# Kernel tuning notes

Hardware: AMD Instinct MI355X
Metric: run time of the kernel (lower is better)

## Reference

```python
import jax, jax.numpy as jnp
import numpy as np

B, C, H, W, K = 4, 96, 56, 56, 9
CM = 2 * C  # graph-conv output channels (standard Grapher: 2*in_channels)


def setup_inputs() -> dict:
    key = jax.random.key(0)
    ks = jax.random.split(key, 6)
    x = jax.random.normal(ks[0], (B, C, H, W), jnp.float32)
    fc1_w = jax.random.normal(ks[1], (C, C), jnp.float32) * 0.05
    fc1_b = jnp.zeros((C,), jnp.float32)
    gconv_w = jax.random.normal(ks[2], (CM, 2 * C), jnp.float32) * 0.05
    gconv_b = jnp.zeros((CM,), jnp.float32)
    fc2_w = jax.random.normal(ks[3], (C, CM), jnp.float32) * 0.05
    fc2_b = jnp.zeros((C,), jnp.float32)
    sa_w = jax.random.normal(ks[4], (1, 2, 7, 7), jnp.float32) * 0.05
    return dict(x=x, fc1_w=fc1_w, fc1_b=fc1_b, gconv_w=gconv_w, gconv_b=gconv_b,
                fc2_w=fc2_w, fc2_b=fc2_b, sa_w=sa_w)


def _knn_idx(xf, k):
    # xf: (B, C, N) -> (B, N, k) nearest-neighbor indices (includes self),
    # matching dense_knn_matrix: topk of negative squared euclidean distance.
    x2 = jnp.sum(xf * xf, axis=1)                       # (B, N)
    inner = jnp.einsum('bcn,bcm->bnm', xf, xf)          # (B, N, N)
    dist = x2[:, :, None] - 2.0 * inner + x2[:, None, :]
    _, idx = jax.lax.top_k(-dist, k)                    # (B, N, k)
    return idx


def _grapher(x, fc1_w, fc1_b, gconv_w, gconv_b, fc2_w, fc2_b, sa_w):
    shortcut = x
    # fc1: 1x1 conv C -> C
    h = jnp.einsum('bchw,oc->bohw', x, fc1_w) + fc1_b[None, :, None, None]
    b, c, hh, ww = h.shape
    n = hh * ww
    xf = h.reshape(b, c, n)                              # nodes: (B, C, N)
    idx = _knn_idx(xf, K)                                # dynamic KNN graph
    # EdgeConv2d: gather x_j at neighbor indices, x_i = center
    xt = jnp.transpose(xf, (0, 2, 1))                    # (B, N, C)
    x_j = jax.vmap(lambda t, i: t[i])(xt, idx)           # (B, N, K, C)
    x_j = jnp.transpose(x_j, (0, 3, 1, 2))               # (B, C, N, K)
    x_i = xf[:, :, :, None]                              # (B, C, N, 1)
    feat = jnp.concatenate(
        [jnp.broadcast_to(x_i, x_j.shape), x_j - x_i], axis=1)  # (B, 2C, N, K)
    e = jnp.einsum('bcnk,oc->bonk', feat, gconv_w) + gconv_b[None, :, None, None]
    e = jax.nn.relu(e)
    g = jnp.max(e, axis=-1)                              # max over K neighbors
    g = g.reshape(b, CM, hh, ww)
    # fc2: 1x1 conv 2C -> C
    out = jnp.einsum('bchw,oc->bohw', g, fc2_w) + fc2_b[None, :, None, None]
    # SpatialAttention: channel mean/max -> 7x7 conv -> sigmoid gate
    avg = jnp.mean(out, axis=1, keepdims=True)
    mx = jnp.max(out, axis=1, keepdims=True)
    sa_in = jnp.concatenate([avg, mx], axis=1)           # (B, 2, H, W)
    att = jax.lax.conv_general_dilated(
        sa_in, sa_w, window_strides=(1, 1), padding=[(3, 3), (3, 3)],
        dimension_numbers=('NCHW', 'OIHW', 'NCHW'))
    att = jax.nn.sigmoid(att)
    return out * att + shortcut


def reference(x, fc1_w, fc1_b, gconv_w, gconv_b, fc2_w, fc2_b, sa_w):
    return _grapher(x, fc1_w, fc1_b, gconv_w, gconv_b, fc2_w, fc2_b, sa_w)
```

## Files before the change

kernel.cpp:

```cpp
#include <hip/hip_runtime.h>

#define BB 4
#define CC 96
#define NN 3136
#define FLTMAX 3.402823466e+38f
#define CAP 44
#define DELTA 1.0f

typedef unsigned short ushort_t;
typedef __attribute__((ext_vector_type(8))) short bf16x8;
typedef __attribute__((ext_vector_type(4))) float f32x4;

__device__ __forceinline__ ushort_t f2bf(float f) {
    unsigned u = __float_as_uint(f);
    unsigned r = (u + 0x7fff + ((u >> 16) & 1)) >> 16;
    return (ushort_t)r;
}
__device__ __forceinline__ float bf2f(ushort_t us) {
    return __uint_as_float(((unsigned)us) << 16);
}


__global__ __launch_bounds__(256) void k_fc1(const float* __restrict__ x, const float* __restrict__ w,
                                             const float* __restrict__ bias, float* __restrict__ h,
                                             float* __restrict__ x2g,
                                             ushort_t* __restrict__ hAhi,
                                             float* __restrict__ hT) {
    __shared__ float sm[96 * 98 + 96 * 64];
    float* wT = sm;
    float* xl = sm + 96 * 98;
    const int tid = threadIdx.x;
    const int n0 = blockIdx.x * 64;
    const int b = blockIdx.y;
    for (int i = tid; i < 96 * 96; i += 256) {
        int o = i / 96, c = i - o * 96;
        wT[c * 98 + o] = w[i];
    }
    const float* xb = x + (size_t)b * CC * NN;
    for (int i = tid; i < 96 * 64; i += 256) {
        int c = i >> 6, nl = i & 63;
        xl[i] = xb[(size_t)c * NN + n0 + nl];
    }
    __syncthreads();
    const int tr = tid >> 4, tc = tid & 15;
    float acc[6][4];
#pragma unroll
    for (int i = 0; i < 6; ++i)
#pragma unroll
        for (int j = 0; j < 4; ++j) acc[i][j] = 0.f;
#pragma unroll 4
    for (int c = 0; c < 96; ++c) {
        float4 xv = *(const float4*)&xl[c * 64 + tc * 4];
        const float* wp = &wT[c * 98 + tr * 6];
        float2 w01 = *(const float2*)(wp);
        float2 w23 = *(const float2*)(wp + 2);
        float2 w45 = *(const float2*)(wp + 4);
        float wv[6] = {w01.x, w01.y, w23.x, w23.y, w45.x, w45.y};
        float xj[4] = {xv.x, xv.y, xv.z, xv.w};
#pragma unroll
        for (int i = 0; i < 6; ++i)
#pragma unroll
            for (int j = 0; j < 4; ++j) acc[i][j] = fmaf(wv[i], xj[j], acc[i][j]);
    }
    float* hb = h + (size_t)b * CC * NN;
    float* hTb = hT + (size_t)b * NN * 96;
    ushort_t* thi = hAhi + (size_t)b * 602112;
#pragma unroll
    for (int i = 0; i < 6; ++i) {
        float bi = bias[tr * 6 + i];
        acc[i][0] += bi; acc[i][1] += bi; acc[i][2] += bi; acc[i][3] += bi;
        float4 o4 = make_float4(acc[i][0], acc[i][1], acc[i][2], acc[i][3]);
        *(float4*)&hb[(size_t)(tr * 6 + i) * NN + n0 + tc * 4] = o4;
        const int c = tr * 6 + i;
        const int cpart = c >> 3;
#pragma unroll
        for (int j = 0; j < 4; ++j) {
            const int n = n0 + tc * 4 + j;
            const int idx = (((n >> 5) * 12 + cpart) * 32 + (n & 31)) * 8 + (c & 7);
            thi[idx] = f2bf(acc[i][j]);
            hTb[(size_t)n * 96 + c] = acc[i][j];
        }
    }
    __syncthreads();
#pragma unroll
    for (int j = 0; j < 4; ++j) {
        float s = 0.f;
#pragma unroll
        for (int i = 0; i < 6; ++i) s = fmaf(acc[i][j], acc[i][j], s);
        sm[tr * 64 + tc * 4 + j] = s;
    }
    __syncthreads();
    if (tid < 64) {
        float s = 0.f;
#pragma unroll
        for (int t = 0; t < 16; ++t) s += sm[t * 64 + tid];
        x2g[(size_t)b * NN + n0 + tid] = s;
    }
}

#define MFMA_TILE_HI(t, acc0, acc1, acc2, acc3)                                       \
    {                                                                                 \
        const int abase_ = (t) * 6144;                                                \
        _Pragma("unroll")                                                             \
        for (int ks_ = 0; ks_ < 3; ++ks_) {                                           \
            const int base_ = abase_ + ks_ * 1024;                                    \
            bf16x8 a0_ = *(const bf16x8*)(hHi + base_ + aoff0);                       \
            bf16x8 a1_ = *(const bf16x8*)(hHi + base_ + aoff1);                       \
            bf16x8 a2_ = *(const bf16x8*)(hHi + base_ + 3072 + aoff0);                \
            bf16x8 a3_ = *(const bf16x8*)(hHi + base_ + 3072 + aoff1);                \
            acc0 = __builtin_amdgcn_mfma_f32_16x16x32_bf16(a0_, bhi[ks_], acc0, 0, 0, 0); \
            acc1 = __builtin_amdgcn_mfma_f32_16x16x32_bf16(a1_, bhi[ks_], acc1, 0, 0, 0); \
            acc2 = __builtin_amdgcn_mfma_f32_16x16x32_bf16(a2_, bhi[ks_], acc2, 0, 0, 0); \
            acc3 = __builtin_amdgcn_mfma_f32_16x16x32_bf16(a3_, bhi[ks_], acc3, 0, 0, 0); \
        }                                                                             \
    }

__global__ __launch_bounds__(256) void k_dist(const ushort_t* __restrict__ hAhi,
                                              const float* __restrict__ x2,
                                              int* __restrict__ cand_cnt,
                                              int* __restrict__ cand_idx,
                                              float* __restrict__ thr_row) {
    __shared__ float thrb[32][24];
    __shared__ float thr_s[32];
    __shared__ int   cnt[32];
    __shared__ int   list[32][CAP];
    const int tid = threadIdx.x;
    const int nb = blockIdx.x, q = blockIdx.y, b = blockIdx.z;
    const int w = tid >> 6, l = tid & 63;
    const int ln = l & 15, lq = l >> 4;
    const int p = w >> 1;
    const int kl_off = lq * 256;
    const ushort_t* hHi = hAhi + (size_t)b * 602112;
    const float* x2b = x2 + (size_t)b * NN;

    const int lane32n = (w & 1) * 16 + ln;
    bf16x8 bhi[3];
#pragma unroll
    for (int ks = 0; ks < 3; ++ks) {
        const int off = nb * 3072 + ks * 1024 + kl_off + lane32n * 8;
        bhi[ks] = *(const bf16x8*)(hHi + off);
    }
    const int aoff0 = kl_off + ln * 8;
    const int aoff1 = kl_off + (16 + ln) * 8;

    const int qb0 = (q == 0) ? 0 : (q == 1) ? 13 : (q == 2) ? 25 : 37;
    const int qb1 = (q == 0) ? 13 : (q == 1) ? 25 : (q == 2) ? 37 : 49;
    const int tstart = qb0 + p;

    unsigned scache[7][8];
    float lv0 = FLTMAX, lv1 = FLTMAX, lv2 = FLTMAX;
#pragma unroll
    for (int ti = 0; ti < 7; ++ti) {
        const int t = tstart + 2 * ti;
        if (t < qb1) {
            const int m0 = t * 64;
            f32x4 acc0 = {0.f, 0.f, 0.f, 0.f}, acc1 = {0.f, 0.f, 0.f, 0.f};
            f32x4 acc2 = {0.f, 0.f, 0.f, 0.f}, acc3 = {0.f, 0.f, 0.f, 0.f};
            MFMA_TILE_HI(t, acc0, acc1, acc2, acc3);
#pragma unroll
            for (int msub = 0; msub < 4; ++msub) {
                f32x4 a = (msub == 0) ? acc0 : (msub == 1) ? acc1 : (msub == 2) ? acc2 : acc3;
                const int mb = m0 + msub * 16 + lq * 4;
                float4 xv = *(const float4*)&x2b[mb];
                float s0 = fmaf(-2.f, a[0], xv.x);
                float s1 = fmaf(-2.f, a[1], xv.y);
                float s2 = fmaf(-2.f, a[2], xv.z);
                float s3 = fmaf(-2.f, a[3], xv.w);
                scache[ti][msub * 2 + 0] = ((unsigned)f2bf(s0) << 16) | (unsigned)f2bf(s1);
                scache[ti][msub * 2 + 1] = ((unsigned)f2bf(s2) << 16) | (unsigned)f2bf(s3);
                float ss[4] = {s0, s1, s2, s3};
#pragma unroll
                for (int r = 0; r < 4; ++r) {
                    float v = ss[r];
                    float t0 = fminf(lv0, v);
                    lv0 = fmaxf(t0, lv1);
                    float t1 = fminf(t0, lv1);
                    lv1 = fmaxf(t1, lv2);
                    lv2 = fminf(t1, lv2);
                }
            }
        }
    }
    {
        const int sidx = (p * 4 + lq) * 3;
        thrb[lane32n][sidx + 0] = lv0;
        thrb[lane32n][sidx + 1] = lv1;
        thrb[lane32n][sidx + 2] = lv2;
    }
    __syncthreads();
    if (tid < 32) {
        float tmp[24];
#pragma unroll
        for (int j = 0; j < 24; ++j) tmp[j] = thrb[tid][j];
        float last = FLTMAX;
        for (int kk = 0; kk < 9; ++kk) {
            float mn = FLTMAX; int ms = 0;
            for (int j = 0; j < 24; ++j)
                if (tmp[j] < mn) { mn = tmp[j]; ms = j; }
            tmp[ms] = FLTMAX;
            last = mn;
        }
        thr_s[tid] = last + DELTA;
        cnt[tid] = 0;
        thr_row[((size_t)b * NN + nb * 32 + tid) * 4 + q] = last + DELTA;
    }
    __syncthreads();
    const float thr = thr_s[lane32n];

#pragma unroll
    for (int ti = 0; ti < 7; ++ti) {
        const int t = tstart + 2 * ti;
        if (t < qb1) {
            const int m0 = t * 64;
#pragma unroll
            for (int msub = 0; msub < 4; ++msub) {
                const int mb = m0 + msub * 16 + lq * 4;
                const unsigned u01 = scache[ti][msub * 2 + 0];
                const unsigned u23 = scache[ti][msub * 2 + 1];
                unsigned bits[4] = {u01 >> 16, u01 & 0xffffu, u23 >> 16, u23 & 0xffffu};
#pragma unroll
                for (int r = 0; r < 4; ++r) {
                    if (bf2f((ushort_t)bits[r]) <= thr) {
                        int pos = atomicAdd(&cnt[lane32n], 1);
                        if (pos < CAP) list[lane32n][pos] = (int)((bits[r] << 16) | (unsigned)(mb + r));
                    }
                }
            }
        }
    }
    __syncthreads();
    const size_t rowbase = (size_t)b * NN + nb * 32;
    if (tid < 32) cand_cnt[(rowbase + tid) * 4 + q] = min(cnt[tid], CAP);
    for (int i = tid; i < 32 * CAP; i += 256) {
        int r = i / CAP, j = i - r * CAP;
        if (j < min(cnt[r], CAP))
            cand_idx[((rowbase + r) * 4 + q) * CAP + j] = list[r][j];
    }
}

__global__ __launch_bounds__(256) void k_merge9(const int* __restrict__ cand_cnt,
                                                const int* __restrict__ cand_idx,
                                                const float* __restrict__ thr_row,
                                                const float* __restrict__ hT,
                                                const float* __restrict__ x2,
                                                int* __restrict__ idx9) {
    __shared__ int  np[4];
    __shared__ int2 pl[4][192];
    const int tid = threadIdx.x;
    const int wv = tid >> 6, lane = tid & 63;
    const size_t n = (size_t)blockIdx.x * 4 + wv;
    const int b = (int)(n / NN);
    const int nn = (int)(n - (size_t)b * NN);
    const int c0 = cand_cnt[n * 4 + 0];
    const int c1 = cand_cnt[n * 4 + 1];
    const int c2 = cand_cnt[n * 4 + 2];
    const int c3 = cand_cnt[n * 4 + 3];
    const int p1 = c0, p2 = c0 + c1, p3 = c0 + c1 + c2;
    const int ct = p3 + c3;
    const float cutoff = fminf(fminf(thr_row[n * 4 + 0], thr_row[n * 4 + 1]),
                               fminf(thr_row[n * 4 + 2], thr_row[n * 4 + 3]));
    if (lane == 0) np[wv] = 0;
    const float* hTb = hT + (size_t)b * NN * 96;
    const float* own = hTb + (size_t)nn * 96;
    const float* x2b = x2 + (size_t)b * NN;
#pragma unroll
    for (int t = 0; t < 3; ++t) {
        const int j = lane + 64 * t;
        if (j < ct) {
            const int qq = (j >= p1) + (j >= p2) + (j >= p3);
            const int base = (qq == 0) ? 0 : (qq == 1) ? p1 : (qq == 2) ? p2 : p3;
            const unsigned u = (unsigned)cand_idx[(n * 4 + qq) * CAP + (j - base)];
            const float av = bf2f((ushort_t)(u >> 16));
            if (av <= cutoff) {
                const int cj = (int)(u & 0xffffu);
                const float* cr = hTb + (size_t)cj * 96;
                float dot = 0.f;
#pragma unroll
                for (int i = 0; i < 24; ++i) {
                    float4 rv = *(const float4*)&own[i * 4];
                    float4 cv4 = *(const float4*)&cr[i * 4];
                    dot = fmaf(rv.x, cv4.x, dot);
                    dot = fmaf(rv.y, cv4.y, dot);
                    dot = fmaf(rv.z, cv4.z, dot);
                    dot = fmaf(rv.w, cv4.w, dot);
                }
                const float v = fmaf(-2.f, dot, x2b[cj]);
                const int pos = atomicAdd(&np[wv], 1);
                pl[wv][pos] = make_int2(__float_as_int(v), cj);
            }
        }
    }
    const int npw = np[wv];
    int2 mine[3]; int rk[3];
#pragma unroll
    for (int t = 0; t < 3; ++t) {
        const int s = lane + 64 * t;
        mine[t] = (s < npw) ? pl[wv][s] : make_int2(0x7f7fffff, 0x7fffffff);
        rk[t] = 0;
    }
    for (int j2 = 0; j2 < npw; ++j2) {
        const int2 e = pl[wv][j2];
        const float ev = __int_as_float(e.x);
#pragma unroll
        for (int t = 0; t < 3; ++t) {
            const float mv = __int_as_float(mine[t].x);
            rk[t] += (ev < mv || (ev == mv && e.y < mine[t].y)) ? 1 : 0;
        }
    }
    int* dst = idx9 + n * 9;
#pragma unroll
    for (int t = 0; t < 3; ++t) {
        const int s = lane + 64 * t;
        if (s < npw && rk[t] < 9) dst[rk[t]] = mine[t].y;
    }
}

__global__ __launch_bounds__(256) void k_ac(const float* __restrict__ h, const float* __restrict__ gw,
                                            const float* __restrict__ gb, ushort_t* __restrict__ acT) {
    __shared__ float sm[96 * 98 + 96 * 64];
    float* wT = sm;
    float* hl = sm + 96 * 98;
    const int tid = threadIdx.x;
    const int n0 = blockIdx.x * 64, ot = blockIdx.y, b = blockIdx.z;
    for (int i = tid; i < 96 * 96; i += 256) {
        int o = i / 96, c = i - o * 96;
        float v;
        if (ot < 2) {
            const float* gwp = gw + (size_t)(ot * 96 + o) * 192;
            v = gwp[c] - gwp[96 + c];
        } else {
            v = gw[(size_t)((ot - 2) * 96 + o) * 192 + 96 + c];
        }
        wT[c * 98 + o] = v;
    }
    const float* hb = h + (size_t)b * CC * NN;
    for (int i = tid; i < 96 * 64; i += 256) {
        int c = i >> 6, nl = i & 63;
        hl[i] = hb[(size_t)c * NN + n0 + nl];
    }
    __syncthreads();
    const int tr = tid >> 4, tc = tid & 15;
    float acc[6][4];
#pragma unroll
    for (int i = 0; i < 6; ++i)
#pragma unroll
        for (int j = 0; j < 4; ++j) acc[i][j] = 0.f;
#pragma unroll 4
    for (int c = 0; c < 96; ++c) {
        float4 xv = *(const float4*)&hl[c * 64 + tc * 4];
        const float* wp = &wT[c * 98 + tr * 6];
        float2 w01 = *(const float2*)(wp);
        float2 w23 = *(const float2*)(wp + 2);
        float2 w45 = *(const float2*)(wp + 4);
        float wv[6] = {w01.x, w01.y, w23.x, w23.y, w45.x, w45.y};
        float xj[4] = {xv.x, xv.y, xv.z, xv.w};
#pragma unroll
        for (int i = 0; i < 6; ++i)
#pragma unroll
            for (int j = 0; j < 4; ++j) acc[i][j] = fmaf(wv[i], xj[j], acc[i][j]);
    }
    const int obase = ot * 96 + tr * 6;
    float bs[6];
#pragma unroll
    for (int i = 0; i < 6; ++i) bs[i] = (ot < 2) ? gb[obase + i] : 0.f;
#pragma unroll
    for (int j = 0; j < 4; ++j) {
        ushort_t* dst = acT + ((size_t)b * NN + n0 + tc * 4 + j) * 384 + obase;
        ushort2 p0, p1, p2;
        p0.x = f2bf(acc[0][j] + bs[0]); p0.y = f2bf(acc[1][j] + bs[1]);
        p1.x = f2bf(acc[2][j] + bs[2]); p1.y = f2bf(acc[3][j] + bs[3]);
        p2.x = f2bf(acc[4][j] + bs[4]); p2.y = f2bf(acc[5][j] + bs[5]);
        *(ushort2*)(dst + 0) = p0;
        *(ushort2*)(dst + 2) = p1;
        *(ushort2*)(dst + 4) = p2;
    }
}

__global__ __launch_bounds__(256) void k_gather(const ushort_t* __restrict__ acT,
                                                const int* __restrict__ idx9,
                                                float* __restrict__ gT) {
    const int lane = threadIdx.x & 63;
    const int wv = threadIdx.x >> 6;
    const int b = blockIdx.y;
    const int nb = blockIdx.x * 16 + wv * 4;
    for (int r = 0; r < 4; ++r) {
        const int n = nb + r;
        const ushort_t* ar = acT + ((size_t)b * NN + n) * 384;
        float a0 = bf2f(ar[lane]), a1 = bf2f(ar[lane + 64]), a2 = bf2f(ar[lane + 128]);
        const int* ip = idx9 + ((size_t)b * NN + n) * 9;
        int jj[9];
#pragma unroll
        for (int k = 0; k < 9; ++k) jj[k] = ip[k];
        float m0 = -FLTMAX, m1 = -FLTMAX, m2 = -FLTMAX;
#pragma unroll
        for (int k = 0; k < 9; ++k) {
            const ushort_t* cr = acT + ((size_t)b * NN + jj[k]) * 384 + 192;
            m0 = fmaxf(m0, a0 + bf2f(cr[lane]));
            m1 = fmaxf(m1, a1 + bf2f(cr[lane + 64]));
            m2 = fmaxf(m2, a2 + bf2f(cr[lane + 128]));
        }
        float* gr = gT + ((size_t)b * NN + n) * 192;
        gr[lane] = fmaxf(m0, 0.f);
        gr[lane + 64] = fmaxf(m1, 0.f);
        gr[lane + 128] = fmaxf(m2, 0.f);
    }
}

__global__ __launch_bounds__(256) void k_fc2(const float* __restrict__ gT, const float* __restrict__ w,
                                             const float* __restrict__ bias, float* __restrict__ out,
                                             float* __restrict__ sa_in) {
    __shared__ float Wc[96 * 36];
    __shared__ float Gc[16 * 36];
    __shared__ float red[2][16][17];
    const int tid = threadIdx.x;
    const int n0 = blockIdx.x * 16, b = blockIdx.y;
    const int tr = tid >> 4, tc = tid & 15;
    float acc[6];
#pragma unroll
    for (int i = 0; i < 6; ++i) acc[i] = 0.f;
    for (int kc = 0; kc < 192; kc += 32) {
        for (int i = tid; i < 96 * 32; i += 256) {
            int c = i >> 5, k = i & 31;
            Wc[c * 36 + k] = w[(size_t)c * 192 + kc + k];
        }
        for (int i = tid; i < 16 * 32; i += 256) {
            int nl = i >> 5, k = i & 31;
            Gc[nl * 36 + k] = gT[((size_t)b * NN + n0 + nl) * 192 + kc + k];
        }
        __syncthreads();
#pragma unroll
        for (int k = 0; k < 32; k += 4) {
            float4 gv = *(const float4*)&Gc[tc * 36 + k];
#pragma unroll
            for (int i = 0; i < 6; ++i) {
                float4 wv = *(const float4*)&Wc[(tr * 6 + i) * 36 + k];
                acc[i] = fmaf(wv.x, gv.x, acc[i]);
                acc[i] = fmaf(wv.y, gv.y, acc[i]);
                acc[i] = fmaf(wv.z, gv.z, acc[i]);
                acc[i] = fmaf(wv.w, gv.w, acc[i]);
            }
        }
        __syncthreads();
    }
    float* ob = out + (size_t)b * CC * NN;
    float ps = 0.f, pm = -FLTMAX;
#pragma unroll
    for (int i = 0; i < 6; ++i) {
        float o = acc[i] + bias[tr * 6 + i];
        ob[(size_t)(tr * 6 + i) * NN + n0 + tc] = o;
        ps += o;
        pm = fmaxf(pm, o);
    }
    red[0][tr][tc] = ps;
    red[1][tr][tc] = pm;
    __syncthreads();
    if (tid < 16) {
        float s_ = 0.f, m_ = -FLTMAX;
#pragma unroll
        for (int t = 0; t < 16; ++t) { s_ += red[0][t][tid]; m_ = fmaxf(m_, red[1][t][tid]); }
        sa_in[(size_t)b * 2 * NN + n0 + tid] = s_ * (1.0f / 96.0f);
        sa_in[(size_t)b * 2 * NN + NN + n0 + tid] = m_;
    }
}

__global__ __launch_bounds__(256) void k_att(const float* __restrict__ sa_in, const float* __restrict__ sw,
                                             const float* __restrict__ x, float* __restrict__ out) {
    int n = blockIdx.x * 256 + threadIdx.x;
    int b = blockIdx.y;
    if (n >= NN) return;
    int y = n / 56, xw = n - y * 56;
    float acc = 0.f;
#pragma unroll
    for (int ci = 0; ci < 2; ++ci) {
        const float* sb = sa_in + ((size_t)b * 2 + ci) * NN;
#pragma unroll
        for (int dy = 0; dy < 7; ++dy) {
            int yy = y + dy - 3;
            if ((unsigned)yy < 56u) {
#pragma unroll
                for (int dx = 0; dx < 7; ++dx) {
                    int xx = xw + dx - 3;
                    if ((unsigned)xx < 56u)
                        acc = fmaf(sb[yy * 56 + xx], sw[(ci * 7 + dy) * 7 + dx], acc);
                }
            }
        }
    }
    float att = 1.f / (1.f + expf(-acc));
    const float* xb = x + (size_t)b * CC * NN + n;
    float* ob = out + (size_t)b * CC * NN + n;
#pragma unroll 4
    for (int c = 0; c < 96; ++c) {
        size_t o = (size_t)c * NN;
        ob[o] = fmaf(ob[o], att, xb[o]);
    }
}

extern "C" void kernel_launch(void* const* d_in, const int* in_sizes, int n_in,
                              void* d_out, int out_size, void* d_ws, size_t ws_size,
                              hipStream_t stream) {
    (void)in_sizes; (void)n_in; (void)out_size; (void)ws_size;
    const float* x       = (const float*)d_in[0];
    const float* fc1_w   = (const float*)d_in[1];
    const float* fc1_b   = (const float*)d_in[2];
    const float* gconv_w = (const float*)d_in[3];
    const float* gconv_b = (const float*)d_in[4];
    const float* fc2_w   = (const float*)d_in[5];
    const float* fc2_b   = (const float*)d_in[6];
    const float* sa_w    = (const float*)d_in[7];
    float* out = (float*)d_out;

    float* ws   = (float*)d_ws;
    float* h    = ws;
    float* x2   = h + (size_t)BB * CC * NN;
    int*   idx9 = (int*)(x2 + BB * NN);
    float* regA = (float*)(idx9 + (size_t)BB * NN * 9);
    ushort_t* hAhi = (ushort_t*)regA;
    ushort_t* acT  = (ushort_t*)regA;
    float* hT   = regA + 2408448;
    float* regB = hT + 1204224;
    int*   cand_idx = (int*)regB;
    int*   cand_cnt = (int*)(regB + 2207744);
    float* thr_row  = regB + 2207744 + 50176;
    float* gT   = regB;
    float* sa_in = regB + 2408448;

    k_fc1   <<<dim3(49, BB), 256, 0, stream>>>(x, fc1_w, fc1_b, h, x2, hAhi, hT);
    k_dist  <<<dim3(98, 4, BB), 256, 0, stream>>>(hAhi, x2, cand_cnt, cand_idx, thr_row);
    k_merge9<<<dim3(3136), 256, 0, stream>>>(cand_cnt, cand_idx, thr_row, hT, x2, idx9);
    k_ac    <<<dim3(49, 4, BB), 256, 0, stream>>>(h, gconv_w, gconv_b, acT);
    k_gather<<<dim3(196, BB), 256, 0, stream>>>(acT, idx9, gT);
    k_fc2   <<<dim3(196, BB), 256, 0, stream>>>(gT, fc2_w, fc2_b, out, sa_in);
    k_att   <<<dim3(13, BB), 256, 0, stream>>>(sa_in, sa_w, x, out);
}
```

Baseline: 248.2 us.

## Split candidate distance dot products across four lanes in KNN merge

The merge kernel now first compacts the surviving candidate indices into shared memory, then recomputes their distances with four lanes per candidate. Each lane handles 24 channels and the partial sums are combined with xor shuffles. Previously each active lane serially read a full 96-float row, which gave divergent, poorly coalesced loads. The change adds block-wide barriers and a loop bounded by the largest wave's candidate count, so waves with fewer candidates sit idle through extra iterations.

```diff
diff --git a/kernel.cpp b/kernel.cpp
--- a/kernel.cpp
+++ b/kernel.cpp
@@ -245,7 +245,8 @@
                                                 const float* __restrict__ x2,
                                                 int* __restrict__ idx9) {
     __shared__ int  np[4];
-    __shared__ int2 pl[4][192];
+    __shared__ int  cl[4][192];
+    __shared__ int2 vl[4][192];
     const int tid = threadIdx.x;
     const int wv = tid >> 6, lane = tid & 63;
     const size_t n = (size_t)blockIdx.x * 4 + wv;
@@ -260,9 +261,7 @@
     const float cutoff = fminf(fminf(thr_row[n * 4 + 0], thr_row[n * 4 + 1]),
                                fminf(thr_row[n * 4 + 2], thr_row[n * 4 + 3]));
     if (lane == 0) np[wv] = 0;
-    const float* hTb = hT + (size_t)b * NN * 96;
-    const float* own = hTb + (size_t)nn * 96;
-    const float* x2b = x2 + (size_t)b * NN;
+    __syncthreads();
 #pragma unroll
     for (int t = 0; t < 3; ++t) {
         const int j = lane + 64 * t;
@@ -272,34 +271,57 @@
             const unsigned u = (unsigned)cand_idx[(n * 4 + qq) * CAP + (j - base)];
             const float av = bf2f((ushort_t)(u >> 16));
             if (av <= cutoff) {
-                const int cj = (int)(u & 0xffffu);
-                const float* cr = hTb + (size_t)cj * 96;
-                float dot = 0.f;
-#pragma unroll
-                for (int i = 0; i < 24; ++i) {
-                    float4 rv = *(const float4*)&own[i * 4];
-                    float4 cv4 = *(const float4*)&cr[i * 4];
-                    dot = fmaf(rv.x, cv4.x, dot);
-                    dot = fmaf(rv.y, cv4.y, dot);
-                    dot = fmaf(rv.z, cv4.z, dot);
-                    dot = fmaf(rv.w, cv4.w, dot);
-                }
-                const float v = fmaf(-2.f, dot, x2b[cj]);
                 const int pos = atomicAdd(&np[wv], 1);
-                pl[wv][pos] = make_int2(__float_as_int(v), cj);
+                cl[wv][pos] = (int)(u & 0xffffu);
             }
         }
     }
+    __syncthreads();
     const int npw = np[wv];
+    const int npmax = max(max(np[0], np[1]), max(np[2], np[3]));
+    const float* hTb = hT + (size_t)b * NN * 96;
+    const float* x2b = x2 + (size_t)b * NN;
+    const int part = lane & 3, slot = lane >> 2;
+    float4 ro[6];
+    {
+        const float* own = hTb + (size_t)nn * 96 + part * 24;
+#pragma unroll
+        for (int i = 0; i < 6; ++i) ro[i] = *(const float4*)&own[i * 4];
+    }
+    for (int base = 0; base < npmax; base += 16) {
+        const int s = base + slot;
+        const bool act = (s < npw);
+        int cj = 0;
+        float dot = 0.f;
+        if (act) {
+            cj = cl[wv][s];
+            const float* cr = hTb + (size_t)cj * 96 + part * 24;
+#pragma unroll
+            for (int i = 0; i < 6; ++i) {
+                float4 cv = *(const float4*)&cr[i * 4];
+                dot = fmaf(ro[i].x, cv.x, dot);
+                dot = fmaf(ro[i].y, cv.y, dot);
+                dot = fmaf(ro[i].z, cv.z, dot);
+                dot = fmaf(ro[i].w, cv.w, dot);
+            }
+        }
+        dot += __shfl_xor(dot, 1, 64);
+        dot += __shfl_xor(dot, 2, 64);
+        if (act && part == 0) {
+            const float v = fmaf(-2.f, dot, x2b[cj]);
+            vl[wv][s] = make_int2(__float_as_int(v), cj);
+        }
+    }
+    __syncthreads();
     int2 mine[3]; int rk[3];
 #pragma unroll
     for (int t = 0; t < 3; ++t) {
         const int s = lane + 64 * t;
-        mine[t] = (s < npw) ? pl[wv][s] : make_int2(0x7f7fffff, 0x7fffffff);
+        mine[t] = (s < npw) ? vl[wv][s] : make_int2(0x7f7fffff, 0x7fffffff);
         rk[t] = 0;
     }
     for (int j2 = 0; j2 < npw; ++j2) {
-        const int2 e = pl[wv][j2];
+        const int2 e = vl[wv][j2];
         const float ev = __int_as_float(e.x);
 #pragma unroll
         for (int t = 0; t < 3; ++t) {
```

Measured after the change: 227.5 us. -8.4%, faster.
